# Performance work log

Measured on AMD Instinct MI355X. Metric: run time of the kernel, lower is better.

## Reference

```python
import jax, jax.numpy as jnp
import numpy as np

B, C, S, D = 4, 16, 512, 512
H = 8
HD = D // H
FFN = 2048
MAX_WL = 10000.0
ROPE_PCT = 0.5
EPS = 1e-5


def setup_inputs() -> dict:
    key = jax.random.key(0)
    ks = jax.random.split(key, 8)
    w = lambda k, shape: jax.random.normal(k, shape, jnp.float32) * 0.02
    return {
        "x": jax.random.normal(ks[0], (B, C, S, D), jnp.float32),
        "Wq": w(ks[1], (D, D)), "bq": jnp.zeros((D,), jnp.float32),
        "Wk": w(ks[2], (D, D)), "bk": jnp.zeros((D,), jnp.float32),
        "Wv": w(ks[3], (D, D)), "bv": jnp.zeros((D,), jnp.float32),
        "Wo": w(ks[4], (D, D)), "bo": jnp.zeros((D,), jnp.float32),
        "ln1_g": jnp.ones((D,), jnp.float32), "ln1_b": jnp.zeros((D,), jnp.float32),
        "ln3_g": jnp.ones((D,), jnp.float32), "ln3_b": jnp.zeros((D,), jnp.float32),
        "W1": w(ks[5], (D, FFN)), "b1": jnp.zeros((FFN,), jnp.float32),
        "W2": w(ks[6], (FFN, D)), "b2": jnp.zeros((D,), jnp.float32),
    }


def _layernorm(x, g, b):
    mu = jnp.mean(x, axis=-1, keepdims=True)
    var = jnp.mean((x - mu) ** 2, axis=-1, keepdims=True)
    return (x - mu) * jax.lax.rsqrt(var + EPS) * g + b


def _p_rope(x, pos):
    # partial rotary: rotate first ROPE_PCT fraction of rotation angles, pass rest through
    half = HD // 2
    rope_angles = int(ROPE_PCT * HD) // 2  # 16 for HD=64, pct=0.5
    exps = (2.0 / HD) * jnp.arange(rope_angles, dtype=jnp.float32)
    timescale = MAX_WL ** exps
    timescale = jnp.concatenate([timescale, jnp.full((half - rope_angles,), jnp.inf, jnp.float32)])
    ang = pos[:, None] / timescale[None, :]  # (S, half); inf timescale -> angle 0 -> identity
    sin, cos = jnp.sin(ang), jnp.cos(ang)
    x1, x2 = x[..., :half], x[..., half:]
    return jnp.concatenate([x1 * cos - x2 * sin, x2 * cos + x1 * sin], axis=-1)


def _forward(x, Wq, bq, Wk, bk, Wv, bv, Wo, bo, ln1_g, ln1_b, ln3_g, ln3_b, W1, b1, W2, b2):
    h = x.reshape(B * C, S, D)
    # --- temporal self-attention (pre-norm) ---
    hn = _layernorm(h, ln1_g, ln1_b)
    scaling = HD ** -0.5
    q = (hn @ Wq + bq) * scaling
    k = hn @ Wk + bk
    v = hn @ Wv + bv
    split = lambda t: t.reshape(B * C, S, H, HD).transpose(0, 2, 1, 3)  # (BC,H,S,HD)
    q, k, v = split(q), split(k), split(v)
    pos = jnp.arange(S, dtype=jnp.float32)
    q = _p_rope(q, pos)
    k = _p_rope(k, pos)
    attn = jax.nn.softmax(jnp.einsum('bhqd,bhkd->bhqk', q, k), axis=-1)
    o = jnp.einsum('bhqk,bhkd->bhqd', attn, v)
    o = o.transpose(0, 2, 1, 3).reshape(B * C, S, D) @ Wo + bo
    h = h + o
    # --- feed-forward (pre-norm) ---
    hn = _layernorm(h, ln3_g, ln3_b)
    ff = jax.nn.gelu(hn @ W1 + b1, approximate=False) @ W2 + b2
    h = h + ff
    return h.reshape(B, C, S, D)


def reference(x, Wq, bq, Wk, bk, Wv, bv, Wo, bo, ln1_g, ln1_b, ln3_g, ln3_b, W1, b1, W2, b2):
    return _forward(x, Wq, bq, Wk, bk, Wv, bv, Wo, bo, ln1_g, ln1_b, ln3_g, ln3_b, W1, b1, W2, b2)
```

## Files before the change

### kernel.cpp

```cpp
#include <hip/hip_runtime.h>
#include <math.h>

typedef unsigned short u16;
typedef __attribute__((ext_vector_type(8))) short bf16x8;
typedef __attribute__((ext_vector_type(4))) float f32x4;

#define MFMA16(a, b, c) __builtin_amdgcn_mfma_f32_16x16x32_bf16((a), (b), (c), 0, 0, 0)

__device__ __forceinline__ u16 f2bf(float f) {
    union { float f; unsigned u; } v; v.f = f;
    unsigned u = v.u;
    unsigned r = (u + 0x7FFFu + ((u >> 16) & 1u)) >> 16;
    return (u16)r;
}

__device__ __forceinline__ unsigned pack_bf16(float lo, float hi) {
    union { float f; unsigned u; } a, b; a.f = lo; b.f = hi;
    return __builtin_amdgcn_perm(b.u + 0x8000u, a.u + 0x8000u, 0x07060302u);
}

__device__ __forceinline__ float fexp2(float x) {
#if __has_builtin(__builtin_amdgcn_exp2f)
    return __builtin_amdgcn_exp2f(x);
#else
    return __expf(x * 0.6931471805599453f);
#endif
}

__device__ __forceinline__ void gl_lds16(const u16* g, u16* l) {
    __builtin_amdgcn_global_load_lds(
        (const __attribute__((address_space(1))) unsigned*)g,
        (__attribute__((address_space(3))) unsigned*)l, 16, 0, 0);
}

__global__ __launch_bounds__(256) void transpose_cvt(const float* __restrict__ src,
                                                     u16* __restrict__ dst, int K, int N) {
    __shared__ float tile[64][65];
    int n0 = blockIdx.x * 64, k0 = blockIdx.y * 64;
    int tx = threadIdx.x & 63, ty = threadIdx.x >> 6;
    #pragma unroll
    for (int i = ty; i < 64; i += 4)
        tile[i][tx] = src[(size_t)(k0 + i) * N + n0 + tx];
    __syncthreads();
    #pragma unroll
    for (int i = ty; i < 64; i += 4)
        dst[(size_t)(n0 + i) * K + k0 + tx] = f2bf(tile[tx][i]);
}

__global__ __launch_bounds__(256) void ln_kernel(const float* __restrict__ in,
                                                 u16* __restrict__ out,
                                                 const float* __restrict__ g,
                                                 const float* __restrict__ b) {
    int row = blockIdx.x;
    const float* rp = in + (size_t)row * 512;
    int t = threadIdx.x;
    float2 v = *(const float2*)(rp + t * 2);
    float s = v.x + v.y;
    float sq = v.x * v.x + v.y * v.y;
    #pragma unroll
    for (int off = 32; off > 0; off >>= 1) {
        s  += __shfl_down(s, off, 64);
        sq += __shfl_down(sq, off, 64);
    }
    __shared__ float red[8];
    __shared__ float stat[2];
    int wid = t >> 6;
    if ((t & 63) == 0) { red[wid] = s; red[wid + 4] = sq; }
    __syncthreads();
    if (t == 0) {
        float S = red[0] + red[1] + red[2] + red[3];
        float Q = red[4] + red[5] + red[6] + red[7];
        float mu = S * (1.0f / 512.0f);
        float var = Q * (1.0f / 512.0f) - mu * mu;
        stat[0] = mu;
        stat[1] = rsqrtf(var + 1e-5f);
    }
    __syncthreads();
    float mu = stat[0], inv = stat[1];
    int c = t * 2;
    float2 gv = *(const float2*)(g + c);
    float2 bv = *(const float2*)(b + c);
    ushort2 ov;
    ov.x = f2bf((v.x - mu) * inv * gv.x + bv.x);
    ov.y = f2bf((v.y - mu) * inv * gv.y + bv.y);
    *(ushort2*)(out + (size_t)row * 512 + c) = ov;
}

__global__ __launch_bounds__(256) void qkv_kernel(
    const u16* __restrict__ A,
    const u16* __restrict__ wqt, const u16* __restrict__ wkt, const u16* __restrict__ wvt,
    const float* __restrict__ bqp, const float* __restrict__ bkp, const float* __restrict__ bvp,
    u16* __restrict__ qb, u16* __restrict__ kb, u16* __restrict__ vb, float sclq)
{
    __shared__ u16 lA[2][128 * 32];
    __shared__ u16 lB[2][128 * 32];
    const int K = 512;
    int flat = blockIdx.y * gridDim.x + blockIdx.x;
    int xcd = flat & 7, slot = flat >> 3;
    int mt = xcd * 32 + slot / 12;
    int nt = slot % 12;
    int mode = nt >> 2;
    int m0 = mt * 128, n0 = (nt & 3) * 128;
    const u16* Bt = (mode == 0) ? wqt : (mode == 1) ? wkt : wvt;
    const float* bias = (mode == 0) ? bqp : (mode == 1) ? bkp : bvp;
    u16* outp = (mode == 0) ? qb : (mode == 1) ? kb : vb;

    int t = threadIdx.x;
    int wid = t >> 6, lane = t & 63, lm = lane & 15, lq = lane >> 4;
    int wm = (wid >> 1) * 64, wn = (wid & 1) * 64;
    const f32x4 zero = {0.f, 0.f, 0.f, 0.f};
    f32x4 acc[4][4];
    #pragma unroll
    for (int i = 0; i < 4; ++i)
        #pragma unroll
        for (int j = 0; j < 4; ++j) acc[i][j] = zero;

    int rr = t >> 2, cc = (t & 3) * 8;
    const u16* Ab = A + (size_t)(m0 + rr) * K + cc;
    const u16* Bb = Bt + (size_t)(n0 + rr) * K + cc;
    size_t pstep = (size_t)64 * K;
    int ldst = t * 8;

    for (int k0 = 0; k0 < K; k0 += 64) {
        #pragma unroll
        for (int h = 0; h < 2; ++h)
            #pragma unroll
            for (int p = 0; p < 2; ++p) {
                gl_lds16(Ab + k0 + h * 32 + p * pstep, lA[h] + p * 2048 + ldst);
                gl_lds16(Bb + k0 + h * 32 + p * pstep, lB[h] + p * 2048 + ldst);
            }
        __syncthreads();
        #pragma unroll
        for (int h = 0; h < 2; ++h) {
            bf16x8 af[4], bg[4];
            #pragma unroll
            for (int i = 0; i < 4; ++i) af[i] = *(const bf16x8*)&lA[h][(wm + i * 16 + lm) * 32 + lq * 8];
            #pragma unroll
            for (int i = 0; i < 4; ++i) bg[i] = *(const bf16x8*)&lB[h][(wn + i * 16 + lm) * 32 + lq * 8];
            #pragma unroll
            for (int i = 0; i < 4; ++i)
                #pragma unroll
                for (int j = 0; j < 4; ++j)
                    acc[i][j] = MFMA16(af[i], bg[j], acc[i][j]);
        }
        __syncthreads();
    }

    if (mode < 2) {
        float bv0 = bias[n0 + wn + 0 * 16 + lm];
        float bv1 = bias[n0 + wn + 1 * 16 + lm];
        float bv2 = bias[n0 + wn + 2 * 16 + lm];
        float bv3 = bias[n0 + wn + 3 * 16 + lm];
        float its = __expf((float)lm * -0.28782313662425572f);
        float scl = (mode == 0) ? sclq : 1.f;
        #pragma unroll
        for (int i = 0; i < 4; ++i) {
            #pragma unroll
            for (int r = 0; r < 4; ++r) {
                int gm = m0 + wm + i * 16 + lq * 4 + r;
                int s = gm & 511;
                float ang = (float)s * its;
                float sn = __sinf(ang), cs = __cosf(ang);
                float x1 = acc[i][0][r] + bv0;
                float x2 = acc[i][2][r] + bv2;
                float y0 = (x1 * cs - x2 * sn) * scl;
                float y2 = (x2 * cs + x1 * sn) * scl;
                float y1 = (acc[i][1][r] + bv1) * scl;
                float y3 = (acc[i][3][r] + bv3) * scl;
                size_t base = ((size_t)(gm >> 9)) * 262144 + (size_t)((n0 + wn) >> 6) * 32768
                            + (size_t)s * 64 + lm;
                outp[base +  0] = f2bf(y0);
                outp[base + 16] = f2bf(y1);
                outp[base + 32] = f2bf(y2);
                outp[base + 48] = f2bf(y3);
            }
        }
    } else {
        #pragma unroll
        for (int i = 0; i < 4; ++i) {
            #pragma unroll
            for (int j = 0; j < 4; ++j) {
                int gn = n0 + wn + j * 16 + lm;
                float bvv = bias[gn];
                #pragma unroll
                for (int r = 0; r < 4; ++r) {
                    int gm = m0 + wm + i * 16 + lq * 4 + r;
                    float v = acc[i][j][r] + bvv;
                    size_t idx = ((size_t)(gm >> 9)) * 262144 + (size_t)(gn >> 6) * 32768
                               + (size_t)(gn & 63) * 512 + (gm & 511);
                    outp[idx] = f2bf(v);
                }
            }
        }
    }
}

template<int MODE>
__global__ __launch_bounds__(256) void gemm_kernel(
    const u16* __restrict__ A, const u16* __restrict__ Bt,
    const float* __restrict__ bias, const float* __restrict__ res,
    void* __restrict__ outp, int M, int N, int K)
{
    __shared__ u16 lA[2][128 * 32];
    __shared__ u16 lB[2][128 * 32];
    int flat = blockIdx.y * gridDim.x + blockIdx.x;
    int xcd = flat & 7, slot = flat >> 3;
    int nb = gridDim.x;
    int mper = gridDim.y >> 3;
    int mt = xcd * mper + slot / nb;
    int nt = slot % nb;
    int m0 = mt * 128, n0 = nt * 128;

    int t = threadIdx.x;
    int wid = t >> 6, lane = t & 63, lm = lane & 15, lq = lane >> 4;
    int wm = (wid >> 1) * 64, wn = (wid & 1) * 64;
    const f32x4 zero = {0.f, 0.f, 0.f, 0.f};
    f32x4 acc[4][4];
    #pragma unroll
    for (int i = 0; i < 4; ++i)
        #pragma unroll
        for (int j = 0; j < 4; ++j) acc[i][j] = zero;

    int rr = t >> 2, cc = (t & 3) * 8;
    const u16* Ab = A + (size_t)(m0 + rr) * K + cc;
    const u16* Bb = Bt + (size_t)(n0 + rr) * K + cc;
    size_t pstep = (size_t)64 * K;
    int ldst = t * 8;

    for (int k0 = 0; k0 < K; k0 += 64) {
        #pragma unroll
        for (int h = 0; h < 2; ++h)
            #pragma unroll
            for (int p = 0; p < 2; ++p) {
                gl_lds16(Ab + k0 + h * 32 + p * pstep, lA[h] + p * 2048 + ldst);
                gl_lds16(Bb + k0 + h * 32 + p * pstep, lB[h] + p * 2048 + ldst);
            }
        __syncthreads();
        #pragma unroll
        for (int h = 0; h < 2; ++h) {
            bf16x8 af[4], bg[4];
            #pragma unroll
            for (int i = 0; i < 4; ++i) af[i] = *(const bf16x8*)&lA[h][(wm + i * 16 + lm) * 32 + lq * 8];
            #pragma unroll
            for (int i = 0; i < 4; ++i) bg[i] = *(const bf16x8*)&lB[h][(wn + i * 16 + lm) * 32 + lq * 8];
            #pragma unroll
            for (int i = 0; i < 4; ++i)
                #pragma unroll
                for (int j = 0; j < 4; ++j)
                    acc[i][j] = MFMA16(af[i], bg[j], acc[i][j]);
        }
        __syncthreads();
    }

    #pragma unroll
    for (int i = 0; i < 4; ++i) {
        #pragma unroll
        for (int j = 0; j < 4; ++j) {
            int gn = n0 + wn + j * 16 + lm;
            float bv = bias[gn];
            #pragma unroll
            for (int r = 0; r < 4; ++r) {
                int gm = m0 + wm + i * 16 + lq * 4 + r;
                float v = acc[i][j][r] + bv;
                if (MODE == 3) {
                    size_t idx = (size_t)gm * N + gn;
                    ((float*)outp)[idx] = v + res[idx];
                } else {
                    float gl = 0.5f * v * (1.f + erff(v * 0.70710678118654752f));
                    ((u16*)outp)[(size_t)gm * N + gn] = f2bf(gl);
                }
            }
        }
    }
}

__global__ __launch_bounds__(256) void attn_kernel(
    const u16* __restrict__ q, const u16* __restrict__ k,
    const u16* __restrict__ vt, u16* __restrict__ o)
{
    int flat = blockIdx.y * gridDim.x + blockIdx.x;
    int xcd = flat & 7, slot = flat >> 3;
    int nh = xcd * 64 + (slot >> 3);
    int qt = slot & 7;
    const u16* Qb = q + (size_t)nh * 32768 + (size_t)qt * 4096;
    const u16* Kb = k + (size_t)nh * 32768;
    const u16* Vb = vt + (size_t)nh * 32768;
    __shared__ u16 lQ[64][72], lK[64][72], lV[64][72];
    __shared__ u16 lP[4][16][72];
    int t = threadIdx.x, wid = t >> 6, lane = t & 63, lm = lane & 15, lq = lane >> 4;

    #pragma unroll
    for (int p = 0; p < 2; ++p) {
        int idx = p * 256 + t, row = idx >> 3, ch = (idx & 7) * 8;
        *(uint4*)&lQ[row][ch] = *(const uint4*)(Qb + (size_t)row * 64 + ch);
    }
    const f32x4 zero = {0.f, 0.f, 0.f, 0.f};
    f32x4 Oacc[4];
    #pragma unroll
    for (int i = 0; i < 4; ++i) Oacc[i] = zero;
    float mo = -INFINITY, l = 0.f;

    for (int kt = 0; kt < 8; ++kt) {
        #pragma unroll
        for (int p = 0; p < 2; ++p) {
            int idx = p * 256 + t, row = idx >> 3, ch = (idx & 7) * 8;
            *(uint4*)&lK[row][ch] = *(const uint4*)(Kb + (size_t)(kt * 64 + row) * 64 + ch);
            *(uint4*)&lV[row][ch] = *(const uint4*)(Vb + (size_t)row * 512 + kt * 64 + ch);
        }
        __syncthreads();
        bf16x8 bq0 = *(const bf16x8*)&lQ[wid * 16 + lm][lq * 8];
        bf16x8 bq1 = *(const bf16x8*)&lQ[wid * 16 + lm][32 + lq * 8];
        f32x4 sc[4];
        #pragma unroll
        for (int i = 0; i < 4; ++i) {
            bf16x8 a0 = *(const bf16x8*)&lK[i * 16 + lm][lq * 8];
            bf16x8 a1 = *(const bf16x8*)&lK[i * 16 + lm][32 + lq * 8];
            f32x4 z = MFMA16(a0, bq0, zero);
            sc[i] = MFMA16(a1, bq1, z);
        }
        float mx = sc[0][0];
        #pragma unroll
        for (int i = 0; i < 4; ++i)
            #pragma unroll
            for (int r = 0; r < 4; ++r) mx = fmaxf(mx, sc[i][r]);
        mx = fmaxf(mx, __shfl_xor(mx, 16, 64));
        mx = fmaxf(mx, __shfl_xor(mx, 32, 64));
        float mn = fmaxf(mo, mx);
        float al = fexp2(mo - mn);
        float pv[4][4], sum = 0.f;
        #pragma unroll
        for (int i = 0; i < 4; ++i)
            #pragma unroll
            for (int r = 0; r < 4; ++r) { pv[i][r] = fexp2(sc[i][r] - mn); sum += pv[i][r]; }
        sum += __shfl_xor(sum, 16, 64);
        sum += __shfl_xor(sum, 32, 64);
        l = l * al + sum;
        mo = mn;
        #pragma unroll
        for (int dn = 0; dn < 4; ++dn) Oacc[dn] *= al;
        #pragma unroll
        for (int i = 0; i < 4; ++i) {
            uint2 w2;
            w2.x = pack_bf16(pv[i][0], pv[i][1]);
            w2.y = pack_bf16(pv[i][2], pv[i][3]);
            *(uint2*)&lP[wid][lm][i * 16 + lq * 4] = w2;
        }
        bf16x8 bp0 = *(const bf16x8*)&lP[wid][lm][lq * 8];
        bf16x8 bp1 = *(const bf16x8*)&lP[wid][lm][32 + lq * 8];
        #pragma unroll
        for (int dn = 0; dn < 4; ++dn) {
            bf16x8 a0 = *(const bf16x8*)&lV[dn * 16 + lm][lq * 8];
            bf16x8 a1 = *(const bf16x8*)&lV[dn * 16 + lm][32 + lq * 8];
            Oacc[dn] = MFMA16(a0, bp0, Oacc[dn]);
            Oacc[dn] = MFMA16(a1, bp1, Oacc[dn]);
        }
        __syncthreads();
    }
    int bc = nh >> 3, h = nh & 7;
    float inv = 1.f / l;
    size_t orow = ((size_t)(bc * 512 + qt * 64 + wid * 16 + lm)) * 512 + h * 64;
    #pragma unroll
    for (int dn = 0; dn < 4; ++dn) {
        uint2 w2;
        w2.x = pack_bf16(Oacc[dn][0] * inv, Oacc[dn][1] * inv);
        w2.y = pack_bf16(Oacc[dn][2] * inv, Oacc[dn][3] * inv);
        *(uint2*)(o + orow + dn * 16 + lq * 4) = w2;
    }
}

extern "C" void kernel_launch(void* const* d_in, const int* in_sizes, int n_in,
                              void* d_out, int out_size, void* d_ws, size_t ws_size,
                              hipStream_t stream) {
    const float* x    = (const float*)d_in[0];
    const float* Wq   = (const float*)d_in[1];
    const float* bq   = (const float*)d_in[2];
    const float* Wk   = (const float*)d_in[3];
    const float* bk   = (const float*)d_in[4];
    const float* Wv   = (const float*)d_in[5];
    const float* bv   = (const float*)d_in[6];
    const float* Wo   = (const float*)d_in[7];
    const float* bo   = (const float*)d_in[8];
    const float* ln1g = (const float*)d_in[9];
    const float* ln1b = (const float*)d_in[10];
    const float* ln3g = (const float*)d_in[11];
    const float* ln3b = (const float*)d_in[12];
    const float* W1   = (const float*)d_in[13];
    const float* b1   = (const float*)d_in[14];
    const float* W2   = (const float*)d_in[15];
    const float* b2   = (const float*)d_in[16];

    char* ws = (char*)d_ws;
    u16*  hn  = (u16*)(ws + 0ull);
    u16*  qb  = (u16*)(ws + 33554432ull);
    u16*  kb  = (u16*)(ws + 67108864ull);
    u16*  vb  = (u16*)(ws + 100663296ull);
    u16*  ob  = (u16*)(ws + 134217728ull);
    u16*  ffa = (u16*)(ws + 33554432ull);
    float* h1 = (float*)(ws + 167772160ull);
    u16*  wqt = (u16*)(ws + 234881024ull);
    u16*  wkt = (u16*)(ws + 235405312ull);
    u16*  wvt = (u16*)(ws + 235929600ull);
    u16*  wot = (u16*)(ws + 236453888ull);
    u16*  w1t = (u16*)(ws + 236978176ull);
    u16*  w2t = (u16*)(ws + 239075328ull);

    dim3 blk(256);
    transpose_cvt<<<dim3(8, 8),  blk, 0, stream>>>(Wq, wqt, 512, 512);
    transpose_cvt<<<dim3(8, 8),  blk, 0, stream>>>(Wk, wkt, 512, 512);
    transpose_cvt<<<dim3(8, 8),  blk, 0, stream>>>(Wv, wvt, 512, 512);
    transpose_cvt<<<dim3(8, 8),  blk, 0, stream>>>(Wo, wot, 512, 512);
    transpose_cvt<<<dim3(32, 8), blk, 0, stream>>>(W1, w1t, 512, 2048);
    transpose_cvt<<<dim3(8, 32), blk, 0, stream>>>(W2, w2t, 2048, 512);

    ln_kernel<<<32768, blk, 0, stream>>>(x, hn, ln1g, ln1b);

    qkv_kernel<<<dim3(12, 256), blk, 0, stream>>>(hn, wqt, wkt, wvt, bq, bk, bv,
                                                  qb, kb, vb, 0.125f * 1.4426950408889634f);

    attn_kernel<<<dim3(8, 512), blk, 0, stream>>>(qb, kb, vb, ob);

    gemm_kernel<3><<<dim3(4, 256), blk, 0, stream>>>(ob, wot, bo, x, h1, 32768, 512, 512);

    ln_kernel<<<32768, blk, 0, stream>>>(h1, hn, ln3g, ln3b);

    gemm_kernel<4><<<dim3(16, 256), blk, 0, stream>>>(hn, w1t, b1, nullptr, ffa, 32768, 2048, 512);
    gemm_kernel<3><<<dim3(4, 256), blk, 0, stream>>>(ffa, w2t, b2, h1, (float*)d_out, 32768, 512, 2048);
}
```

Measured before the change: 658.3 us.

## Process four query tiles per attention block and merge weight transposes

The attention kernel now handles 256 query rows per block instead of 64. Q fragments are held in registers, and each K/V tile staged in LDS (plus its fragments) is reused across four query sub-tiles, which cuts redundant K/V global and LDS traffic by a factor of four. In exchange the block count drops to a quarter and register pressure rises from the per-subtile accumulators, which may lower occupancy. Separately, the six weight transpose launches are merged into one kernel to reduce launch overhead.

```diff
diff --git a/kernel.cpp b/kernel.cpp
--- a/kernel.cpp
+++ b/kernel.cpp
@@ -33,10 +33,27 @@
         (__attribute__((address_space(3))) unsigned*)l, 16, 0, 0);
 }
 
-__global__ __launch_bounds__(256) void transpose_cvt(const float* __restrict__ src,
-                                                     u16* __restrict__ dst, int K, int N) {
+__global__ __launch_bounds__(256) void transpose_cvt_all(
+    const float* __restrict__ Wq, const float* __restrict__ Wk,
+    const float* __restrict__ Wv, const float* __restrict__ Wo,
+    const float* __restrict__ W1, const float* __restrict__ W2,
+    u16* __restrict__ wqt, u16* __restrict__ wkt, u16* __restrict__ wvt,
+    u16* __restrict__ wot, u16* __restrict__ w1t, u16* __restrict__ w2t)
+{
     __shared__ float tile[64][65];
-    int n0 = blockIdx.x * 64, k0 = blockIdx.y * 64;
+    int fb = blockIdx.x;
+    const float* src; u16* dst; int K, N, bx, by;
+    if (fb < 256) {
+        int w = fb >> 6, b = fb & 63;
+        src = (w == 0) ? Wq : (w == 1) ? Wk : (w == 2) ? Wv : Wo;
+        dst = (w == 0) ? wqt : (w == 1) ? wkt : (w == 2) ? wvt : wot;
+        K = 512; N = 512; bx = b & 7; by = b >> 3;
+    } else if (fb < 512) {
+        int b = fb - 256; src = W1; dst = w1t; K = 512; N = 2048; bx = b & 31; by = b >> 5;
+    } else {
+        int b = fb - 512; src = W2; dst = w2t; K = 2048; N = 512; bx = b & 7; by = b >> 3;
+    }
+    int n0 = bx * 64, k0 = by * 64;
     int tx = threadIdx.x & 63, ty = threadIdx.x >> 6;
     #pragma unroll
     for (int i = ty; i < 64; i += 4)
@@ -280,25 +297,32 @@
 {
     int flat = blockIdx.y * gridDim.x + blockIdx.x;
     int xcd = flat & 7, slot = flat >> 3;
-    int nh = xcd * 64 + (slot >> 3);
-    int qt = slot & 7;
-    const u16* Qb = q + (size_t)nh * 32768 + (size_t)qt * 4096;
+    int nh = xcd * 64 + (slot >> 1);
+    int qt = slot & 1;
+    const u16* Qb = q + (size_t)nh * 32768 + (size_t)qt * 16384;
     const u16* Kb = k + (size_t)nh * 32768;
     const u16* Vb = vt + (size_t)nh * 32768;
-    __shared__ u16 lQ[64][72], lK[64][72], lV[64][72];
+    __shared__ u16 lK[64][72], lV[64][72];
     __shared__ u16 lP[4][16][72];
     int t = threadIdx.x, wid = t >> 6, lane = t & 63, lm = lane & 15, lq = lane >> 4;
 
-    #pragma unroll
-    for (int p = 0; p < 2; ++p) {
-        int idx = p * 256 + t, row = idx >> 3, ch = (idx & 7) * 8;
-        *(uint4*)&lQ[row][ch] = *(const uint4*)(Qb + (size_t)row * 64 + ch);
-    }
+    bf16x8 bq[4][2];
+    #pragma unroll
+    for (int sub = 0; sub < 4; ++sub) {
+        const u16* qr = Qb + (size_t)(sub * 64 + wid * 16 + lm) * 64;
+        bq[sub][0] = *(const bf16x8*)(qr + lq * 8);
+        bq[sub][1] = *(const bf16x8*)(qr + 32 + lq * 8);
+    }
+
     const f32x4 zero = {0.f, 0.f, 0.f, 0.f};
-    f32x4 Oacc[4];
-    #pragma unroll
-    for (int i = 0; i < 4; ++i) Oacc[i] = zero;
-    float mo = -INFINITY, l = 0.f;
+    f32x4 Oacc[4][4];
+    float mo[4], l[4];
+    #pragma unroll
+    for (int s = 0; s < 4; ++s) {
+        mo[s] = -INFINITY; l[s] = 0.f;
+        #pragma unroll
+        for (int d = 0; d < 4; ++d) Oacc[s][d] = zero;
+    }
 
     for (int kt = 0; kt < 8; ++kt) {
         #pragma unroll
@@ -308,63 +332,71 @@
             *(uint4*)&lV[row][ch] = *(const uint4*)(Vb + (size_t)row * 512 + kt * 64 + ch);
         }
         __syncthreads();
-        bf16x8 bq0 = *(const bf16x8*)&lQ[wid * 16 + lm][lq * 8];
-        bf16x8 bq1 = *(const bf16x8*)&lQ[wid * 16 + lm][32 + lq * 8];
-        f32x4 sc[4];
+        bf16x8 aK[4][2], aV[4][2];
         #pragma unroll
         for (int i = 0; i < 4; ++i) {
-            bf16x8 a0 = *(const bf16x8*)&lK[i * 16 + lm][lq * 8];
-            bf16x8 a1 = *(const bf16x8*)&lK[i * 16 + lm][32 + lq * 8];
-            f32x4 z = MFMA16(a0, bq0, zero);
-            sc[i] = MFMA16(a1, bq1, z);
-        }
-        float mx = sc[0][0];
-        #pragma unroll
-        for (int i = 0; i < 4; ++i)
-            #pragma unroll
-            for (int r = 0; r < 4; ++r) mx = fmaxf(mx, sc[i][r]);
-        mx = fmaxf(mx, __shfl_xor(mx, 16, 64));
-        mx = fmaxf(mx, __shfl_xor(mx, 32, 64));
-        float mn = fmaxf(mo, mx);
-        float al = fexp2(mo - mn);
-        float pv[4][4], sum = 0.f;
-        #pragma unroll
-        for (int i = 0; i < 4; ++i)
-            #pragma unroll
-            for (int r = 0; r < 4; ++r) { pv[i][r] = fexp2(sc[i][r] - mn); sum += pv[i][r]; }
-        sum += __shfl_xor(sum, 16, 64);
-        sum += __shfl_xor(sum, 32, 64);
-        l = l * al + sum;
-        mo = mn;
-        #pragma unroll
-        for (int dn = 0; dn < 4; ++dn) Oacc[dn] *= al;
-        #pragma unroll
-        for (int i = 0; i < 4; ++i) {
+            aK[i][0] = *(const bf16x8*)&lK[i * 16 + lm][lq * 8];
+            aK[i][1] = *(const bf16x8*)&lK[i * 16 + lm][32 + lq * 8];
+            aV[i][0] = *(const bf16x8*)&lV[i * 16 + lm][lq * 8];
+            aV[i][1] = *(const bf16x8*)&lV[i * 16 + lm][32 + lq * 8];
+        }
+        #pragma unroll
+        for (int sub = 0; sub < 4; ++sub) {
+            f32x4 sc[4];
+            #pragma unroll
+            for (int i = 0; i < 4; ++i) {
+                f32x4 z = MFMA16(aK[i][0], bq[sub][0], zero);
+                sc[i] = MFMA16(aK[i][1], bq[sub][1], z);
+            }
+            float mx = sc[0][0];
+            #pragma unroll
+            for (int i = 0; i < 4; ++i)
+                #pragma unroll
+                for (int r = 0; r < 4; ++r) mx = fmaxf(mx, sc[i][r]);
+            mx = fmaxf(mx, __shfl_xor(mx, 16, 64));
+            mx = fmaxf(mx, __shfl_xor(mx, 32, 64));
+            float mn = fmaxf(mo[sub], mx);
+            float al = fexp2(mo[sub] - mn);
+            float pv[4][4], sum = 0.f;
+            #pragma unroll
+            for (int i = 0; i < 4; ++i)
+                #pragma unroll
+                for (int r = 0; r < 4; ++r) { pv[i][r] = fexp2(sc[i][r] - mn); sum += pv[i][r]; }
+            sum += __shfl_xor(sum, 16, 64);
+            sum += __shfl_xor(sum, 32, 64);
+            l[sub] = l[sub] * al + sum;
+            mo[sub] = mn;
+            #pragma unroll
+            for (int dn = 0; dn < 4; ++dn) Oacc[sub][dn] *= al;
+            #pragma unroll
+            for (int i = 0; i < 4; ++i) {
+                uint2 w2;
+                w2.x = pack_bf16(pv[i][0], pv[i][1]);
+                w2.y = pack_bf16(pv[i][2], pv[i][3]);
+                *(uint2*)&lP[wid][lm][i * 16 + lq * 4] = w2;
+            }
+            bf16x8 bp0 = *(const bf16x8*)&lP[wid][lm][lq * 8];
+            bf16x8 bp1 = *(const bf16x8*)&lP[wid][lm][32 + lq * 8];
+            #pragma unroll
+            for (int dn = 0; dn < 4; ++dn) {
+                Oacc[sub][dn] = MFMA16(aV[dn][0], bp0, Oacc[sub][dn]);
+                Oacc[sub][dn] = MFMA16(aV[dn][1], bp1, Oacc[sub][dn]);
+            }
+        }
+        __syncthreads();
+    }
+    int bc = nh >> 3, h = nh & 7;
+    #pragma unroll
+    for (int sub = 0; sub < 4; ++sub) {
+        float inv = 1.f / l[sub];
+        size_t orow = ((size_t)(bc * 512 + qt * 256 + sub * 64 + wid * 16 + lm)) * 512 + h * 64;
+        #pragma unroll
+        for (int dn = 0; dn < 4; ++dn) {
             uint2 w2;
-            w2.x = pack_bf16(pv[i][0], pv[i][1]);
-            w2.y = pack_bf16(pv[i][2], pv[i][3]);
-            *(uint2*)&lP[wid][lm][i * 16 + lq * 4] = w2;
-        }
-        bf16x8 bp0 = *(const bf16x8*)&lP[wid][lm][lq * 8];
-        bf16x8 bp1 = *(const bf16x8*)&lP[wid][lm][32 + lq * 8];
-        #pragma unroll
-        for (int dn = 0; dn < 4; ++dn) {
-            bf16x8 a0 = *(const bf16x8*)&lV[dn * 16 + lm][lq * 8];
-            bf16x8 a1 = *(const bf16x8*)&lV[dn * 16 + lm][32 + lq * 8];
-            Oacc[dn] = MFMA16(a0, bp0, Oacc[dn]);
-            Oacc[dn] = MFMA16(a1, bp1, Oacc[dn]);
-        }
-        __syncthreads();
-    }
-    int bc = nh >> 3, h = nh & 7;
-    float inv = 1.f / l;
-    size_t orow = ((size_t)(bc * 512 + qt * 64 + wid * 16 + lm)) * 512 + h * 64;
-    #pragma unroll
-    for (int dn = 0; dn < 4; ++dn) {
-        uint2 w2;
-        w2.x = pack_bf16(Oacc[dn][0] * inv, Oacc[dn][1] * inv);
-        w2.y = pack_bf16(Oacc[dn][2] * inv, Oacc[dn][3] * inv);
-        *(uint2*)(o + orow + dn * 16 + lq * 4) = w2;
+            w2.x = pack_bf16(Oacc[sub][dn][0] * inv, Oacc[sub][dn][1] * inv);
+            w2.y = pack_bf16(Oacc[sub][dn][2] * inv, Oacc[sub][dn][3] * inv);
+            *(uint2*)(o + orow + dn * 16 + lq * 4) = w2;
+        }
     }
 }
 
@@ -405,19 +437,15 @@
     u16*  w2t = (u16*)(ws + 239075328ull);
 
     dim3 blk(256);
-    transpose_cvt<<<dim3(8, 8),  blk, 0, stream>>>(Wq, wqt, 512, 512);
-    transpose_cvt<<<dim3(8, 8),  blk, 0, stream>>>(Wk, wkt, 512, 512);
-    transpose_cvt<<<dim3(8, 8),  blk, 0, stream>>>(Wv, wvt, 512, 512);
-    transpose_cvt<<<dim3(8, 8),  blk, 0, stream>>>(Wo, wot, 512, 512);
-    transpose_cvt<<<dim3(32, 8), blk, 0, stream>>>(W1, w1t, 512, 2048);
-    transpose_cvt<<<dim3(8, 32), blk, 0, stream>>>(W2, w2t, 2048, 512);
+    transpose_cvt_all<<<768, blk, 0, stream>>>(Wq, Wk, Wv, Wo, W1, W2,
+                                               wqt, wkt, wvt, wot, w1t, w2t);
 
     ln_kernel<<<32768, blk, 0, stream>>>(x, hn, ln1g, ln1b);
 
     qkv_kernel<<<dim3(12, 256), blk, 0, stream>>>(hn, wqt, wkt, wvt, bq, bk, bv,
                                                   qb, kb, vb, 0.125f * 1.4426950408889634f);
 
-    attn_kernel<<<dim3(8, 512), blk, 0, stream>>>(qb, kb, vb, ob);
+    attn_kernel<<<dim3(2, 512), blk, 0, stream>>>(qb, kb, vb, ob);
 
     gemm_kernel<3><<<dim3(4, 256), blk, 0, stream>>>(ob, wot, bo, x, h1, 32768, 512, 512);
 
```

Result: faster. 637.2 us (-3.2%).
